# Performance work log

Hardware: AMD Instinct MI355X
Metric: run time of the kernel (lower is better)

The kernel has to match this reference:

```python
import jax, jax.numpy as jnp
import numpy as np

P = 2; NH = 16; HS = 1024; NL = 12; NC = 1000
B, D, H, W = 32, 64, 32, 32
LFEAT = P * P * D  # 256 per-patch feature dim


def _sincos_1d(dim, pos):
    omega = np.arange(dim // 2, dtype=np.float64) / (dim / 2.0)
    omega = 1.0 / 10000 ** omega
    out = np.einsum('m,d->md', pos.reshape(-1), omega)
    return np.concatenate([np.sin(out), np.cos(out)], axis=1)


def _pos_embed(dim, grid_size):
    g = np.arange(grid_size, dtype=np.float32)
    grid = np.stack(np.meshgrid(g, g), axis=0).reshape(2, 1, grid_size, grid_size)
    emb = np.concatenate([_sincos_1d(dim // 2, grid[0]), _sincos_1d(dim // 2, grid[1])], axis=1)
    return jnp.asarray(emb, dtype=jnp.float32)


def setup_inputs() -> dict:
    key = jax.random.key(0)
    ks = iter(jax.random.split(key, 40))
    def w(shape, s=0.02):
        return jax.random.normal(next(ks), shape, jnp.float32) * s
    return {
        'x': jax.random.normal(next(ks), (B, D, H, W), jnp.float32),
        'y': jax.random.randint(next(ks), (B,), 0, NC),
        't': jax.random.randint(next(ks), (B,), 0, 1000),
        'proj_w': w((LFEAT, HS)), 'proj_b': jnp.zeros((HS,), jnp.float32),
        'pos_embed': _pos_embed(HS, H // P),
        'emb_table': w((NC + 1, HS)),
        'blk_mod_w': w((NL, HS, 6 * HS)), 'blk_mod_b': jnp.zeros((NL, 6 * HS), jnp.float32),
        'blk_wq': w((NL, HS, HS)), 'blk_bq': jnp.zeros((NL, HS), jnp.float32),
        'blk_wk': w((NL, HS, HS)), 'blk_bk': jnp.zeros((NL, HS), jnp.float32),
        'blk_wv': w((NL, HS, HS)), 'blk_bv': jnp.zeros((NL, HS), jnp.float32),
        'blk_wo': w((NL, HS, HS)), 'blk_bo': jnp.zeros((NL, HS), jnp.float32),
        'blk_fc1_w': w((NL, HS, 4 * HS)), 'blk_fc1_b': jnp.zeros((NL, 4 * HS), jnp.float32),
        'blk_fc2_w': w((NL, 4 * HS, HS)), 'blk_fc2_b': jnp.zeros((NL, HS), jnp.float32),
        'fin_mod_w': w((HS, 2 * HS)), 'fin_mod_b': jnp.zeros((2 * HS,), jnp.float32),
        'fin_out_w': w((HS, LFEAT)), 'fin_out_b': jnp.zeros((LFEAT,), jnp.float32),
    }


def _ln(z):
    mu = jnp.mean(z, -1, keepdims=True)
    var = jnp.mean((z - mu) ** 2, -1, keepdims=True)
    return (z - mu) * jax.lax.rsqrt(var + 1e-5)


def _forward(x, y, t, proj_w, proj_b, pos_embed, emb_table,
             blk_mod_w, blk_mod_b, blk_wq, blk_bq, blk_wk, blk_bk, blk_wv, blk_bv,
             blk_wo, blk_bo, blk_fc1_w, blk_fc1_b, blk_fc2_w, blk_fc2_b,
             fin_mod_w, fin_mod_b, fin_out_w, fin_out_b):
    Bc, Dc, Hc, Wc = x.shape
    Hp, Wp = Hc // P, Wc // P
    dh = HS // NH
    # patchify_flatten: (B, L, P*P*D)
    tok = x.reshape(Bc, Dc, Hp, P, Wp, P).transpose(0, 2, 4, 3, 5, 1).reshape(Bc, Hp * Wp, P * P * Dc)
    tok = tok @ proj_w + proj_b + pos_embed[None]
    # timestep_embedding: [cos, sin] order per source
    half = HS // 2
    freqs = jnp.exp(-jnp.log(jnp.float32(10000.0)) * jnp.arange(half, dtype=jnp.float32) / half)
    ang = t.astype(jnp.float32)[:, None] * freqs[None]
    c = jnp.concatenate([jnp.cos(ang), jnp.sin(ang)], axis=-1) + emb_table[y]
    c_act = jax.nn.silu(c)  # each block applies silu to c (c is not mutated across blocks)

    def block(xc, p):
        mw, mb, wq, bq, wk, bk, wv, bv, wo, bo, f1w, f1b, f2w, f2b = p
        mod = c_act @ mw + mb
        sh_a, sc_a, g_a, sh_m, sc_m, g_m = jnp.split(mod, 6, axis=1)
        hx = _ln(xc) * (1 + sc_a[:, None]) + sh_a[:, None]
        def heads(z, wz, bz):
            return (z @ wz + bz).reshape(Bc, -1, NH, dh).transpose(0, 2, 1, 3)
        q, k, v = heads(hx, wq, bq), heads(hx, wk, bk), heads(hx, wv, bv)
        logits = jnp.einsum('bhqd,bhkd->bhqk', q, k) / jnp.sqrt(jnp.float32(dh))
        # non-AR mask buffer is all zeros -> no-op
        attn = jax.nn.softmax(logits, axis=-1)
        o = jnp.einsum('bhqk,bhkd->bhqd', attn, v).transpose(0, 2, 1, 3).reshape(Bc, -1, HS)
        xc = xc + g_a[:, None] * (o @ wo + bo)
        hx = _ln(xc) * (1 + sc_m[:, None]) + sh_m[:, None]
        mlp = jax.nn.gelu(hx @ f1w + f1b, approximate=False) @ f2w + f2b
        return xc + g_m[:, None] * mlp, None

    tok, _ = jax.lax.scan(block, tok, (blk_mod_w, blk_mod_b, blk_wq, blk_bq, blk_wk, blk_bk,
                                       blk_wv, blk_bv, blk_wo, blk_bo,
                                       blk_fc1_w, blk_fc1_b, blk_fc2_w, blk_fc2_b))
    fmod = c_act @ fin_mod_w + fin_mod_b
    sh, sc = jnp.split(fmod, 2, axis=1)
    out = (_ln(tok) * (1 + sc[:, None]) + sh[:, None]) @ fin_out_w + fin_out_b
    # unpatchify -> (B, D, H, W)
    return out.reshape(Bc, Hp, Wp, P, P, Dc).transpose(0, 5, 1, 3, 2, 4).reshape(Bc, Dc, Hc, Wc)


def reference(x, y, t, proj_w, proj_b, pos_embed, emb_table,
              blk_mod_w, blk_mod_b, blk_wq, blk_bq, blk_wk, blk_bk, blk_wv, blk_bv,
              blk_wo, blk_bo, blk_fc1_w, blk_fc1_b, blk_fc2_w, blk_fc2_b,
              fin_mod_w, fin_mod_b, fin_out_w, fin_out_b):
    return _forward(x, y, t, proj_w, proj_b, pos_embed, emb_table,
                    blk_mod_w, blk_mod_b, blk_wq, blk_bq, blk_wk, blk_bk, blk_wv, blk_bv,
                    blk_wo, blk_bo, blk_fc1_w, blk_fc1_b, blk_fc2_w, blk_fc2_b,
                    fin_mod_w, fin_mod_b, fin_out_w, fin_out_b)
```

## Files before the change

kernel.cpp:

```cpp
#include <hip/hip_runtime.h>
#include <hip/hip_bf16.h>
#include <math.h>

typedef short s16x8 __attribute__((ext_vector_type(8)));
typedef float f32x4 __attribute__((ext_vector_type(4)));
typedef unsigned short u16;

__device__ __forceinline__ u16 f2b(float f) {
    unsigned u = __builtin_bit_cast(unsigned, f);
    u += 0x7fffu + ((u >> 16) & 1u);
    return (u16)(u >> 16);
}
__device__ __forceinline__ f32x4 mfma16(s16x8 a, s16x8 b, f32x4 c) {
    return __builtin_amdgcn_mfma_f32_16x16x32_bf16(a, b, c, 0, 0, 0);
}
__device__ __forceinline__ void gload16(const void* g, void* l) {
    __builtin_amdgcn_global_load_lds((const __attribute__((address_space(1))) unsigned*)g,
                                     (__attribute__((address_space(3))) unsigned*)l, 16, 0, 0);
}

__global__ __launch_bounds__(256) void patchify_kernel(const float* __restrict__ x, u16* __restrict__ out) {
    int idx = blockIdx.x * 256 + threadIdx.x;
    int row = idx >> 8, col = idx & 255;
    int b = row >> 8, ll = row & 255, hp = ll >> 4, wp = ll & 15;
    int pp = col >> 6, d = col & 63;
    out[idx] = f2b(x[(size_t)((b * 64 + d) * 32 + hp * 2 + (pp >> 1)) * 32 + wp * 2 + (pp & 1)]);
}

__global__ __launch_bounds__(256) void cact_kernel(const int* __restrict__ t, const int* __restrict__ y,
                                                   const float* __restrict__ emb, float* __restrict__ cactF) {
    int b = blockIdx.x, tid = threadIdx.x;
    float tv = (float)t[b];
    int yb = y[b];
#pragma unroll
    for (int j = 0; j < 4; ++j) {
        int c = tid * 4 + j;
        int f = (c < 512) ? c : c - 512;
        float freq = __expf(-9.210340371976184f * (float)f * (1.f / 512.f));
        float ang = tv * freq;
        float v = (c < 512) ? cosf(ang) : sinf(ang);
        v += emb[(size_t)yb * 1024 + c];
        v = v / (1.f + __expf(-v));
        cactF[b * 1024 + c] = v;
    }
}

__global__ __launch_bounds__(256) void bcat_kernel(const float* __restrict__ bq, const float* __restrict__ bk,
                                                   const float* __restrict__ bv, float* __restrict__ out) {
    int lyr = blockIdx.x, j = blockIdx.y, tid = threadIdx.x;
    const float* src = (j == 0) ? bq : ((j == 1) ? bk : bv);
    float4 v = ((const float4*)(src + (size_t)lyr * 1024))[tid];
    ((float4*)(out + (size_t)lyr * 3072 + j * 1024))[tid] = v;
}

__global__ __launch_bounds__(256) void mod32_kernel(const float* __restrict__ cactF, const float* __restrict__ W,
                                                    const float* __restrict__ bias, float* __restrict__ out, int N) {
    __shared__ float cs[32 * 256];
    __shared__ float red[4 * 32 * 64];
    int tid = threadIdx.x, lane = tid & 63, kg = tid >> 6;
    int n = blockIdx.x * 64 + lane;
    float acc[32];
#pragma unroll
    for (int r = 0; r < 32; ++r) acc[r] = 0.f;
    for (int ch = 0; ch < 4; ++ch) {
        __syncthreads();
#pragma unroll
        for (int j = 0; j < 8; ++j) {
            int idx = tid * 4 + j * 1024;
            float4 v = *(const float4*)&cactF[(size_t)(idx >> 8) * 1024 + ch * 256 + (idx & 255)];
            *(float4*)&cs[idx] = v;
        }
        __syncthreads();
        const float* Wp = W + (size_t)(ch * 256 + kg * 64) * N + n;
        for (int kk = 0; kk < 64; kk += 4) {
            float w0 = Wp[(size_t)(kk + 0) * N];
            float w1 = Wp[(size_t)(kk + 1) * N];
            float w2 = Wp[(size_t)(kk + 2) * N];
            float w3 = Wp[(size_t)(kk + 3) * N];
            int kb = kg * 64 + kk;
#pragma unroll
            for (int r = 0; r < 32; ++r) {
                float4 cv = *(const float4*)&cs[r * 256 + kb];
                acc[r] += cv.x * w0 + cv.y * w1 + cv.z * w2 + cv.w * w3;
            }
        }
    }
#pragma unroll
    for (int r = 0; r < 32; ++r) red[(kg * 32 + r) * 64 + lane] = acc[r];
    __syncthreads();
    int r = tid >> 3, j0 = (tid & 7) * 8;
#pragma unroll
    for (int jj = 0; jj < 8; ++jj) {
        int nn = j0 + jj;
        float s = red[(0 * 32 + r) * 64 + nn] + red[(1 * 32 + r) * 64 + nn] +
                  red[(2 * 32 + r) * 64 + nn] + red[(3 * 32 + r) * 64 + nn];
        out[(size_t)r * N + blockIdx.x * 64 + nn] = s + bias[blockIdx.x * 64 + nn];
    }
}

__device__ __forceinline__ void tpose_body(float (*tile)[65], const float* __restrict__ in,
                                           u16* __restrict__ out, int R, int C, int r0, int c0, int tid) {
    int rr = tid >> 4, cc = (tid & 15) * 4;
#pragma unroll
    for (int j = 0; j < 4; ++j) {
        float4 v = *(const float4*)&in[(size_t)(r0 + j * 16 + rr) * C + c0 + cc];
        tile[j * 16 + rr][cc]     = v.x;
        tile[j * 16 + rr][cc + 1] = v.y;
        tile[j * 16 + rr][cc + 2] = v.z;
        tile[j * 16 + rr][cc + 3] = v.w;
    }
    __syncthreads();
    int oc = tid >> 3, r8 = (tid & 7) * 8;
#pragma unroll
    for (int j = 0; j < 2; ++j) {
        int ocl = j * 32 + oc;
        s16x8 vv;
#pragma unroll
        for (int e = 0; e < 8; ++e) vv[e] = (short)f2b(tile[r8 + e][ocl]);
        *(s16x8*)&out[(size_t)(c0 + ocl) * R + r0 + r8] = vv;
    }
}

__global__ __launch_bounds__(256) void transpose_cvt64k(const float* __restrict__ in, u16* __restrict__ out,
                                                        int R, int C) {
    __shared__ float tile[64][65];
    tpose_body(tile, in, out, R, C, blockIdx.y * 64, blockIdx.x * 64, threadIdx.x);
}

__global__ __launch_bounds__(256) void transpose_layer(
    const float* __restrict__ wq, const float* __restrict__ wk,
    const float* __restrict__ wv, const float* __restrict__ wo, const float* __restrict__ f1,
    const float* __restrict__ f2,
    u16* __restrict__ qkvT, u16* __restrict__ woT, u16* __restrict__ f1T, u16* __restrict__ f2T) {
    __shared__ float tile[64][65];
    int bid = blockIdx.x, tid = threadIdx.x;
    const float* src; u16* dst; int R, C, tloc;
    if (bid < 256)       { src = wq; dst = qkvT;               R = 1024; C = 1024; tloc = bid; }
    else if (bid < 512)  { src = wk; dst = qkvT + 1024 * 1024; R = 1024; C = 1024; tloc = bid - 256; }
    else if (bid < 768)  { src = wv; dst = qkvT + 2048 * 1024; R = 1024; C = 1024; tloc = bid - 512; }
    else if (bid < 1024) { src = wo; dst = woT;                R = 1024; C = 1024; tloc = bid - 768; }
    else if (bid < 2048) { src = f1; dst = f1T;                R = 1024; C = 4096; tloc = bid - 1024; }
    else                 { src = f2; dst = f2T;                R = 4096; C = 1024; tloc = bid - 2048; }
    int tx = C >> 6;
    int ty = tloc / tx, txi = tloc - ty * tx;
    tpose_body(tile, src, dst, R, C, ty * 64, txi * 64, tid);
}

__global__ __launch_bounds__(256) void ln_mod_kernel(const float* __restrict__ x, const float* __restrict__ modv,
                                                     int mod_ld, int sh_off, int sc_off, u16* __restrict__ out) {
    int row = blockIdx.x, tid = threadIdx.x, b = row >> 8;
    float4 xv = ((const float4*)(x + (size_t)row * 1024))[tid];
    float s = xv.x + xv.y + xv.z + xv.w;
    float s2 = xv.x * xv.x + xv.y * xv.y + xv.z * xv.z + xv.w * xv.w;
#pragma unroll
    for (int d = 1; d < 64; d <<= 1) { s += __shfl_xor(s, d); s2 += __shfl_xor(s2, d); }
    __shared__ float red[8];
    int w = tid >> 6;
    if ((tid & 63) == 0) { red[w] = s; red[4 + w] = s2; }
    __syncthreads();
    s = red[0] + red[1] + red[2] + red[3];
    s2 = red[4] + red[5] + red[6] + red[7];
    float mu = s * (1.f / 1024.f);
    float rs = rsqrtf(s2 * (1.f / 1024.f) - mu * mu + 1e-5f);
    const float* shp = modv + (size_t)b * mod_ld + sh_off;
    const float* scp = modv + (size_t)b * mod_ld + sc_off;
    float4 sh4 = ((const float4*)shp)[tid];
    float4 sc4 = ((const float4*)scp)[tid];
    u16 o0 = f2b((xv.x - mu) * rs * (1.f + sc4.x) + sh4.x);
    u16 o1 = f2b((xv.y - mu) * rs * (1.f + sc4.y) + sh4.y);
    u16 o2 = f2b((xv.z - mu) * rs * (1.f + sc4.z) + sh4.z);
    u16 o3 = f2b((xv.w - mu) * rs * (1.f + sc4.w) + sh4.w);
    unsigned long long pk = (unsigned long long)o0 | ((unsigned long long)o1 << 16) |
                            ((unsigned long long)o2 << 32) | ((unsigned long long)o3 << 48);
    *(unsigned long long*)&out[(size_t)row * 1024 + tid * 4] = pk;
}

template <int EPI>
__global__ __launch_bounds__(512, 1) void gemm256(
    const u16* __restrict__ A, int lda, const u16* __restrict__ Bt, int ldb,
    int M, int N, int K, const float* __restrict__ bias, u16* __restrict__ outB, int ldc) {
    __shared__ u16 As[3][256 * 32];
    __shared__ u16 Bs[3][256 * 32];

    const int tid = threadIdx.x, w = tid >> 6, l = tid & 63;
    const int wm = w >> 1, wn = w & 1;
    const int fr = l & 15, fg = l >> 4;

    const int nbn = N >> 8;
    const int orig = blockIdx.x;
    const int cpx = gridDim.x >> 3;
    const int wg = (orig & 7) * cpx + (orig >> 3);
    const int bm = wg / nbn, bn = wg - bm * nbn;
    const int row0 = bm << 8, col0 = bn << 8;
    const int NT = K >> 5;

    const int srow = tid >> 2, slot = tid & 3;
    const int gs = slot ^ ((srow >> 1) & 3);
    const u16* gA = A + (size_t)(row0 + srow) * lda + gs * 8;
    const u16* gB = Bt + (size_t)(col0 + srow) * ldb + gs * 8;

    int aoff[4], boff[8];
#pragma unroll
    for (int m = 0; m < 4; ++m) {
        int rr = wm * 64 + m * 16 + fr;
        aoff[m] = rr * 32 + ((fg ^ ((rr >> 1) & 3)) * 8);
    }
#pragma unroll
    for (int j = 0; j < 8; ++j) {
        int rr = wn * 128 + j * 16 + fr;
        boff[j] = rr * 32 + ((fg ^ ((rr >> 1) & 3)) * 8);
    }

    f32x4 acc[4][8];
#pragma unroll
    for (int m = 0; m < 4; ++m)
#pragma unroll
        for (int j = 0; j < 8; ++j) acc[m][j] = (f32x4){0.f, 0.f, 0.f, 0.f};

    {
        u16* d0 = &As[0][tid * 8];
        gload16(gA, d0); gload16(gA + (size_t)128 * lda, d0 + 4096);
        u16* e0 = &Bs[0][tid * 8];
        gload16(gB, e0); gload16(gB + (size_t)128 * ldb, e0 + 4096);
        u16* d1 = &As[1][tid * 8];
        gload16(gA + 32, d1); gload16(gA + (size_t)128 * lda + 32, d1 + 4096);
        u16* e1 = &Bs[1][tid * 8];
        gload16(gB + 32, e1); gload16(gB + (size_t)128 * ldb + 32, e1 + 4096);
    }
    asm volatile("s_waitcnt vmcnt(4)" ::: "memory");
    __builtin_amdgcn_s_barrier();
    __builtin_amdgcn_sched_barrier(0);

    int q = 0;
    for (int t = 0; t < NT; ++t) {
        const u16* ca = As[q];
        const u16* cb = Bs[q];
        const int q1 = (q == 2) ? 0 : q + 1;
        const int q2 = (q1 == 2) ? 0 : q1 + 1;

        s16x8 af[4], bfv[4];
#pragma unroll
        for (int m = 0; m < 4; ++m) af[m] = *(const s16x8*)(ca + aoff[m]);
#pragma unroll
        for (int j = 0; j < 4; ++j) bfv[j] = *(const s16x8*)(cb + boff[j]);
        if (t + 2 < NT) {
            u16* d = &As[q2][tid * 8];
            const u16* s = gA + (size_t)(t + 2) * 32;
            gload16(s, d); gload16(s + (size_t)128 * lda, d + 4096);
        }
        __builtin_amdgcn_s_barrier();
        __builtin_amdgcn_s_setprio(1);
#pragma unroll
        for (int m = 0; m < 4; ++m)
#pragma unroll
            for (int j = 0; j < 4; ++j) acc[m][j] = mfma16(af[m], bfv[j], acc[m][j]);
        __builtin_amdgcn_s_setprio(0);
        __builtin_amdgcn_s_barrier();
#pragma unroll
        for (int j = 0; j < 4; ++j) bfv[j] = *(const s16x8*)(cb + boff[j + 4]);
        if (t + 2 < NT) {
            u16* d = &Bs[q2][tid * 8];
            const u16* s = gB + (size_t)(t + 2) * 32;
            gload16(s, d); gload16(s + (size_t)128 * ldb, d + 4096);
        }
        __builtin_amdgcn_s_setprio(1);
#pragma unroll
        for (int m = 0; m < 4; ++m)
#pragma unroll
            for (int j = 0; j < 4; ++j) acc[m][j + 4] = mfma16(af[m], bfv[j], acc[m][j + 4]);
        __builtin_amdgcn_s_setprio(0);
        if (t < NT - 2)       { asm volatile("s_waitcnt vmcnt(4)" ::: "memory"); }
        else if (t == NT - 2) { asm volatile("s_waitcnt vmcnt(0)" ::: "memory"); }
        if (t < NT - 1) {
            __builtin_amdgcn_s_barrier();
            __builtin_amdgcn_sched_barrier(0);
        }
        q = q1;
    }

    const int erow = row0 + wm * 64 + fg * 4;
    const int ecol = col0 + wn * 128 + fr;
#pragma unroll
    for (int m = 0; m < 4; ++m) {
#pragma unroll
        for (int j = 0; j < 8; ++j) {
#pragma unroll
            for (int r = 0; r < 4; ++r) {
                int row = erow + m * 16 + r;
                int col = ecol + j * 16;
                float v = acc[m][j][r] + bias[col];
                if constexpr (EPI == 1) {
                    outB[(size_t)row * ldc + col] = f2b(v);
                } else {
                    outB[(size_t)row * ldc + col] = f2b(0.5f * v * (1.f + erff(v * 0.70710678118654752f)));
                }
            }
        }
    }
}

template <int EPI>
__global__ __launch_bounds__(512, 1) void gemm8(
    const u16* __restrict__ A, int lda, const u16* __restrict__ Bt, int ldb,
    int M, int N, int K, const float* __restrict__ bias,
    float* __restrict__ outF, u16* __restrict__ outB, int ldc,
    const float* __restrict__ aux1, const float* __restrict__ aux2, int gateOff) {
    __shared__ u16 As[3][256 * 64];
    __shared__ u16 Bs[3][128 * 64];

    const int tid = threadIdx.x, w = tid >> 6, l = tid & 63;
    const int wm = w >> 1, wn = w & 1;

    const int nbn = N >> 7;
    const int orig = blockIdx.x;
    const int cpx = gridDim.x >> 3;
    const int wg = (orig & 7) * cpx + (orig >> 3);
    const int bm = wg / nbn, bn = wg - bm * nbn;
    const int row0 = bm << 8, col0 = bn << 7;

    const int NT = K >> 6;

    const int srow = tid >> 3, sslot = tid & 7;
    const int ksl = sslot ^ (srow & 7);
    const u16* gA = A + (size_t)(row0 + srow) * lda + ksl * 8;
    const u16* gB = Bt + (size_t)(col0 + srow) * ldb + ksl * 8;
    const int lOff = srow * 64 + sslot * 8;

    const int fr = l & 15, fg = l >> 4;
    const int arow = wm * 64 + fr;
    const int brow = wn * 64 + fr;

    f32x4 acc[4][4];
#pragma unroll
    for (int m = 0; m < 4; ++m)
#pragma unroll
        for (int n = 0; n < 4; ++n) acc[m][n] = (f32x4){0.f, 0.f, 0.f, 0.f};

    {
        u16* a0 = &As[0][lOff];
        u16* b0 = &Bs[0][lOff];
#pragma unroll
        for (int a = 0; a < 4; ++a) gload16(gA + (size_t)a * 64 * lda, a0 + a * 4096);
#pragma unroll
        for (int b = 0; b < 2; ++b) gload16(gB + (size_t)b * 64 * ldb, b0 + b * 4096);
        if (NT > 1) {
            u16* a1 = &As[1][lOff];
#pragma unroll
            for (int a = 0; a < 3; ++a) gload16(gA + (size_t)a * 64 * lda + 64, a1 + a * 4096);
        }
    }
    if (NT > 1) { asm volatile("s_waitcnt vmcnt(3)" ::: "memory"); }
    else        { asm volatile("s_waitcnt vmcnt(0)" ::: "memory"); }
    __builtin_amdgcn_s_barrier();
    __builtin_amdgcn_sched_barrier(0);

    int q = 0;
    for (int t = 0; t < NT; ++t) {
        const u16* ca = As[q];
        const u16* cb = Bs[q];
        const int q1 = (q == 2) ? 0 : q + 1;
        const int q2 = (q1 == 2) ? 0 : q1 + 1;

        s16x8 af[4][2], bf[4][2];
#pragma unroll
        for (int m = 0; m < 4; ++m) {
            int r = arow + m * 16;
            af[m][0] = *(const s16x8*)(ca + r * 64 + ((fg     ^ (r & 7)) * 8));
            af[m][1] = *(const s16x8*)(ca + r * 64 + (((4 + fg) ^ (r & 7)) * 8));
        }
#pragma unroll
        for (int n = 0; n < 2; ++n) {
            int r = brow + n * 16;
            bf[n][0] = *(const s16x8*)(cb + r * 64 + ((fg     ^ (r & 7)) * 8));
            bf[n][1] = *(const s16x8*)(cb + r * 64 + (((4 + fg) ^ (r & 7)) * 8));
        }
        if (t + 1 < NT) {
            gload16(gA + (size_t)(3 * 64) * lda + (size_t)(t + 1) * 64, &As[q1][lOff] + 3 * 4096);
            gload16(gB + (size_t)(t + 1) * 64, &Bs[q1][lOff]);
            gload16(gB + (size_t)(1 * 64) * ldb + (size_t)(t + 1) * 64, &Bs[q1][lOff] + 4096);
        }
        __builtin_amdgcn_s_barrier();
        __builtin_amdgcn_s_setprio(1);
#pragma unroll
        for (int m = 0; m < 4; ++m)
#pragma unroll
            for (int n = 0; n < 2; ++n) {
                acc[m][n] = mfma16(af[m][0], bf[n][0], acc[m][n]);
                acc[m][n] = mfma16(af[m][1], bf[n][1], acc[m][n]);
            }
        __builtin_amdgcn_s_setprio(0);
        __builtin_amdgcn_s_barrier();
#pragma unroll
        for (int n = 0; n < 2; ++n) {
            int r = brow + (n + 2) * 16;
            bf[n + 2][0] = *(const s16x8*)(cb + r * 64 + ((fg     ^ (r & 7)) * 8));
            bf[n + 2][1] = *(const s16x8*)(cb + r * 64 + (((4 + fg) ^ (r & 7)) * 8));
        }
        if (t + 2 < NT) {
#pragma unroll
            for (int a = 0; a < 3; ++a)
                gload16(gA + (size_t)a * 64 * lda + (size_t)(t + 2) * 64, &As[q2][lOff] + a * 4096);
        }
        __builtin_amdgcn_s_barrier();
        __builtin_amdgcn_s_setprio(1);
#pragma unroll
        for (int m = 0; m < 4; ++m)
#pragma unroll
            for (int n = 2; n < 4; ++n) {
                acc[m][n] = mfma16(af[m][0], bf[n][0], acc[m][n]);
                acc[m][n] = mfma16(af[m][1], bf[n][1], acc[m][n]);
            }
        __builtin_amdgcn_s_setprio(0);
        if (t < NT - 2)       { asm volatile("s_waitcnt vmcnt(3)" ::: "memory"); }
        else if (t == NT - 2) { asm volatile("s_waitcnt vmcnt(0)" ::: "memory"); }
        if (t < NT - 1) {
            __builtin_amdgcn_s_barrier();
            __builtin_amdgcn_sched_barrier(0);
        }
        q = q1;
    }

    const int erow = row0 + wm * 64 + fg * 4;
    const int ecol = col0 + wn * 64 + fr;
#pragma unroll
    for (int m = 0; m < 4; ++m) {
#pragma unroll
        for (int n = 0; n < 4; ++n) {
#pragma unroll
            for (int r = 0; r < 4; ++r) {
                int row = erow + m * 16 + r;
                int col = ecol + n * 16;
                float v = acc[m][n][r];
                if constexpr (EPI == 2) {
                    outF[(size_t)row * ldc + col] = v + bias[col] + aux1[(size_t)(row & 255) * 1024 + col];
                } else {
                    outF[(size_t)row * ldc + col] =
                        aux1[(size_t)row * ldc + col] +
                        aux2[(size_t)(row >> 8) * 6144 + gateOff + col] * (v + bias[col]);
                }
            }
        }
    }
}

__global__ __launch_bounds__(256, 2) void gemm_fin(
    const u16* __restrict__ A, int lda, const u16* __restrict__ Bt, int ldb,
    int M, int N, int K, const float* __restrict__ bias, float* outF) {
    __shared__ u16 Asl[128 * 32];
    __shared__ u16 Bsl[128 * 32];
    const int tid = threadIdx.x, w = tid >> 6, l = tid & 63;
    const int row0 = blockIdx.y * 128, col0 = blockIdx.x * 128;
    const int wm = w >> 1, wn = w & 1;

    f32x4 acc[4][4];
#pragma unroll
    for (int m = 0; m < 4; ++m)
#pragma unroll
        for (int n = 0; n < 4; ++n) acc[m][n] = (f32x4){0.f, 0.f, 0.f, 0.f};

    const int rA0 = w * 16 + (l >> 2), rA1 = rA0 + 64;
    const int kc = (l & 3) * 8;
    const u16* a0 = A + (size_t)(row0 + rA0) * lda + kc;
    const u16* a1 = A + (size_t)(row0 + rA1) * lda + kc;
    const u16* b0 = Bt + (size_t)(col0 + rA0) * ldb + kc;
    const u16* b1 = Bt + (size_t)(col0 + rA1) * ldb + kc;
    u16* la0 = &Asl[rA0 * 32 + kc];
    u16* la1 = &Asl[rA1 * 32 + kc];
    u16* lb0 = &Bsl[rA0 * 32 + kc];
    u16* lb1 = &Bsl[rA1 * 32 + kc];

    for (int k0 = 0; k0 < K; k0 += 32) {
        __syncthreads();
        gload16(a0 + k0, la0);
        gload16(a1 + k0, la1);
        gload16(b0 + k0, lb0);
        gload16(b1 + k0, lb1);
        __syncthreads();
        s16x8 af[4], bfr[4];
#pragma unroll
        for (int m = 0; m < 4; ++m)
            af[m] = *(const s16x8*)&Asl[(wm * 64 + m * 16 + (l & 15)) * 32 + (l >> 4) * 8];
#pragma unroll
        for (int n = 0; n < 4; ++n)
            bfr[n] = *(const s16x8*)&Bsl[(wn * 64 + n * 16 + (l & 15)) * 32 + (l >> 4) * 8];
#pragma unroll
        for (int m = 0; m < 4; ++m)
#pragma unroll
            for (int n = 0; n < 4; ++n) acc[m][n] = mfma16(af[m], bfr[n], acc[m][n]);
    }

#pragma unroll
    for (int m = 0; m < 4; ++m) {
#pragma unroll
        for (int n = 0; n < 4; ++n) {
#pragma unroll
            for (int r = 0; r < 4; ++r) {
                int row = row0 + wm * 64 + m * 16 + (l >> 4) * 4 + r;
                int col = col0 + wn * 64 + n * 16 + (l & 15);
                float xg = acc[m][n][r] + bias[col];
                int bb = row >> 8, ll = row & 255, hp = ll >> 4, wp = ll & 15;
                int pp = col >> 6, d = col & 63;
                outF[(size_t)((bb * 64 + d) * 32 + hp * 2 + (pp >> 1)) * 32 + wp * 2 + (pp & 1)] = xg;
            }
        }
    }
}

__global__ __launch_bounds__(256, 2) void attn_kernel(const u16* __restrict__ qkv, u16* __restrict__ obuf) {
    __shared__ u16 Qs[64 * 64];
    __shared__ u16 Ks[256 * 64];
    __shared__ u16 VTs[64 * 256];
    int qt = blockIdx.x, h = blockIdx.y, b = blockIdx.z;
    int tid = threadIdx.x, w = tid >> 6, l = tid & 63;
    size_t base = (size_t)b * 256 * 3072;

    {
        int r = tid >> 2;
#pragma unroll
        for (int j = 0; j < 2; ++j) {
            int sg = (tid & 3) + j * 4;
            *(s16x8*)&Qs[r * 64 + sg * 8] =
                *(const s16x8*)&qkv[base + (size_t)(qt * 64 + r) * 3072 + h * 64 + sg * 8];
        }
    }
#pragma unroll
    for (int j = 0; j < 8; ++j) {
        int i = tid + j * 256;
        int r = i >> 3, sg = i & 7;
        *(s16x8*)&Ks[r * 64 + sg * 8] =
            *(const s16x8*)&qkv[base + (size_t)r * 3072 + 1024 + h * 64 + sg * 8];
    }
#pragma unroll
    for (int j = 0; j < 8; ++j) {
        int i = tid + j * 256;
        int r = i >> 3, sg = i & 7;
        s16x8 v = *(const s16x8*)&qkv[base + (size_t)r * 3072 + 2048 + h * 64 + sg * 8];
#pragma unroll
        for (int e = 0; e < 8; ++e) VTs[(sg * 8 + e) * 256 + r] = ((const u16*)&v)[e];
    }
    __syncthreads();

    s16x8 aq0 = *(const s16x8*)&Qs[(w * 16 + (l & 15)) * 64 + (l >> 4) * 8];
    s16x8 aq1 = *(const s16x8*)&Qs[(w * 16 + (l & 15)) * 64 + 32 + (l >> 4) * 8];
    f32x4 sf[16];
#pragma unroll
    for (int cf = 0; cf < 16; ++cf) {
        f32x4 a = (f32x4){0.f, 0.f, 0.f, 0.f};
        s16x8 bk0 = *(const s16x8*)&Ks[(cf * 16 + (l & 15)) * 64 + (l >> 4) * 8];
        s16x8 bk1 = *(const s16x8*)&Ks[(cf * 16 + (l & 15)) * 64 + 32 + (l >> 4) * 8];
        a = mfma16(aq0, bk0, a);
        a = mfma16(aq1, bk1, a);
        sf[cf] = a * 0.125f;
    }
    __syncthreads();

#pragma unroll
    for (int r = 0; r < 4; ++r) {
        float m = -1e30f;
#pragma unroll
        for (int cf = 0; cf < 16; ++cf) m = fmaxf(m, sf[cf][r]);
#pragma unroll
        for (int d = 1; d < 16; d <<= 1) m = fmaxf(m, __shfl_xor(m, d));
        float sm = 0.f;
#pragma unroll
        for (int cf = 0; cf < 16; ++cf) { float e = __expf(sf[cf][r] - m); sf[cf][r] = e; sm += e; }
#pragma unroll
        for (int d = 1; d < 16; d <<= 1) sm += __shfl_xor(sm, d);
        float inv = 1.f / sm;
        int rl = w * 16 + (l >> 4) * 4 + r;
#pragma unroll
        for (int cf = 0; cf < 16; ++cf) Ks[rl * 256 + cf * 16 + (l & 15)] = f2b(sf[cf][r] * inv);
    }
    __syncthreads();

    f32x4 oacc[4];
#pragma unroll
    for (int cf = 0; cf < 4; ++cf) oacc[cf] = (f32x4){0.f, 0.f, 0.f, 0.f};
#pragma unroll
    for (int ks = 0; ks < 8; ++ks) {
        s16x8 ap = *(const s16x8*)&Ks[(w * 16 + (l & 15)) * 256 + ks * 32 + (l >> 4) * 8];
#pragma unroll
        for (int cf = 0; cf < 4; ++cf) {
            s16x8 bv = *(const s16x8*)&VTs[(cf * 16 + (l & 15)) * 256 + ks * 32 + (l >> 4) * 8];
            oacc[cf] = mfma16(ap, bv, oacc[cf]);
        }
    }
    size_t orow0 = (size_t)(b * 256 + qt * 64 + w * 16);
#pragma unroll
    for (int cf = 0; cf < 4; ++cf)
#pragma unroll
        for (int r = 0; r < 4; ++r) {
            int rr = (l >> 4) * 4 + r;
            obuf[(orow0 + rr) * 1024 + h * 64 + cf * 16 + (l & 15)] = f2b(oacc[cf][r]);
        }
}

extern "C" void kernel_launch(void* const* d_in, const int* in_sizes, int n_in,
                              void* d_out, int out_size, void* d_ws, size_t ws_size,
                              hipStream_t stream) {
    (void)in_sizes; (void)n_in; (void)out_size; (void)ws_size;
    const float* x         = (const float*)d_in[0];
    const int*   y         = (const int*)d_in[1];
    const int*   t         = (const int*)d_in[2];
    const float* proj_w    = (const float*)d_in[3];
    const float* proj_b    = (const float*)d_in[4];
    const float* pos_embed = (const float*)d_in[5];
    const float* emb_table = (const float*)d_in[6];
    const float* blk_mod_w = (const float*)d_in[7];
    const float* blk_mod_b = (const float*)d_in[8];
    const float* blk_wq    = (const float*)d_in[9];
    const float* blk_bq    = (const float*)d_in[10];
    const float* blk_wk    = (const float*)d_in[11];
    const float* blk_bk    = (const float*)d_in[12];
    const float* blk_wv    = (const float*)d_in[13];
    const float* blk_bv    = (const float*)d_in[14];
    const float* blk_wo    = (const float*)d_in[15];
    const float* blk_bo    = (const float*)d_in[16];
    const float* blk_f1w   = (const float*)d_in[17];
    const float* blk_f1b   = (const float*)d_in[18];
    const float* blk_f2w   = (const float*)d_in[19];
    const float* blk_f2b   = (const float*)d_in[20];
    const float* fin_mod_w = (const float*)d_in[21];
    const float* fin_mod_b = (const float*)d_in[22];
    const float* fin_out_w = (const float*)d_in[23];
    const float* fin_out_b = (const float*)d_in[24];
    float* out = (float*)d_out;

    char* ws = (char*)d_ws;
    size_t off = 0;
    auto alloc = [&](size_t bytes) -> char* {
        char* p = ws + off;
        off += (bytes + 255) & ~(size_t)255;
        return p;
    };
    float* xc    = (float*)alloc(8192ull * 1024 * 4);
    u16*   hx    = (u16*)alloc(8192ull * 1024 * 2);
    u16*   qkvb  = (u16*)alloc(8192ull * 3072 * 2);
    u16*   obufp = (u16*)alloc(8192ull * 1024 * 2);
    u16*   h1    = (u16*)alloc(8192ull * 4096 * 2);
    u16*   patchA= (u16*)alloc(8192ull * 256 * 2);
    float* cactF = (float*)alloc(32ull * 1024 * 4);
    float* modb  = (float*)alloc(32ull * 6144 * 4);
    float* fmod  = (float*)alloc(32ull * 2048 * 4);
    float* bqkv  = (float*)alloc(12ull * 3072 * 4);
    u16*   projT = (u16*)alloc(1024ull * 256 * 2);
    u16*   foT   = (u16*)alloc(256ull * 1024 * 2);
    u16*   qkvT  = (u16*)alloc(3072ull * 1024 * 2);
    u16*   woT   = (u16*)alloc(1024ull * 1024 * 2);
    u16*   f1T   = (u16*)alloc(4096ull * 1024 * 2);
    u16*   f2T   = (u16*)alloc(1024ull * 4096 * 2);

    patchify_kernel<<<8192, 256, 0, stream>>>(x, patchA);
    cact_kernel<<<32, 256, 0, stream>>>(t, y, emb_table, cactF);
    bcat_kernel<<<dim3(12, 3), 256, 0, stream>>>(blk_bq, blk_bk, blk_bv, bqkv);
    transpose_cvt64k<<<dim3(16, 4), 256, 0, stream>>>(proj_w, projT, 256, 1024);
    transpose_cvt64k<<<dim3(4, 16), 256, 0, stream>>>(fin_out_w, foT, 1024, 256);
    mod32_kernel<<<32, 256, 0, stream>>>(cactF, fin_mod_w, fin_mod_b, fmod, 2048);

    gemm8<2><<<256, 512, 0, stream>>>(patchA, 256, projT, 256, 8192, 1024, 256,
                                      proj_b, xc, nullptr, 1024, pos_embed, nullptr, 0);

    for (int i = 0; i < 12; ++i) {
        transpose_layer<<<3072, 256, 0, stream>>>(
            blk_wq + (size_t)i * 1024 * 1024, blk_wk + (size_t)i * 1024 * 1024,
            blk_wv + (size_t)i * 1024 * 1024, blk_wo + (size_t)i * 1024 * 1024,
            blk_f1w + (size_t)i * 1024 * 4096, blk_f2w + (size_t)i * 4096 * 1024,
            qkvT, woT, f1T, f2T);

        mod32_kernel<<<96, 256, 0, stream>>>(cactF, blk_mod_w + (size_t)i * 1024 * 6144,
                                             blk_mod_b + (size_t)i * 6144, modb, 6144);
        ln_mod_kernel<<<8192, 256, 0, stream>>>(xc, modb, 6144, 0, 1024, hx);
        gemm256<1><<<384, 512, 0, stream>>>(hx, 1024, qkvT, 1024, 8192, 3072, 1024,
                                            bqkv + (size_t)i * 3072, qkvb, 3072);
        attn_kernel<<<dim3(4, 16, 32), 256, 0, stream>>>(qkvb, obufp);
        gemm8<3><<<256, 512, 0, stream>>>(obufp, 1024, woT, 1024, 8192, 1024, 1024,
                                          blk_bo + (size_t)i * 1024, xc, nullptr, 1024,
                                          xc, modb, 2048);
        ln_mod_kernel<<<8192, 256, 0, stream>>>(xc, modb, 6144, 3072, 4096, hx);
        gemm256<4><<<512, 512, 0, stream>>>(hx, 1024, f1T, 1024, 8192, 4096, 1024,
                                            blk_f1b + (size_t)i * 4096, h1, 4096);
        gemm8<3><<<256, 512, 0, stream>>>(h1, 4096, f2T, 4096, 8192, 1024, 4096,
                                          blk_f2b + (size_t)i * 1024, xc, nullptr, 1024,
                                          xc, modb, 5120);
    }
    ln_mod_kernel<<<8192, 256, 0, stream>>>(xc, fmod, 2048, 0, 1024, hx);
    gemm_fin<<<dim3(2, 64), 256, 0, stream>>>(hx, 1024, foT, 1024, 8192, 256, 1024,
                                              fin_out_b, out);
}
```

Baseline: 6.159 ms.

## Rewrite 256x256 GEMM as 8-phase pipeline with BK=64 and double buffering

```diff
diff --git a/kernel.cpp b/kernel.cpp
--- a/kernel.cpp
+++ b/kernel.cpp
@@ -5,6 +5,12 @@
 typedef short s16x8 __attribute__((ext_vector_type(8)));
 typedef float f32x4 __attribute__((ext_vector_type(4)));
 typedef unsigned short u16;
+
+#define BAR() __builtin_amdgcn_s_barrier()
+#define PRIO1() __builtin_amdgcn_s_setprio(1)
+#define PRIO0() __builtin_amdgcn_s_setprio(0)
+#define VMCNT6() asm volatile("s_waitcnt vmcnt(6)" ::: "memory")
+#define VMCNT0() asm volatile("s_waitcnt vmcnt(0)" ::: "memory")
 
 __device__ __forceinline__ u16 f2b(float f) {
     unsigned u = __builtin_bit_cast(unsigned, f);
@@ -176,14 +182,14 @@
 }
 
 template <int EPI>
-__global__ __launch_bounds__(512, 1) void gemm256(
+__global__ __launch_bounds__(512, 2) void gemm256_8ph(
     const u16* __restrict__ A, int lda, const u16* __restrict__ Bt, int ldb,
     int M, int N, int K, const float* __restrict__ bias, u16* __restrict__ outB, int ldc) {
-    __shared__ u16 As[3][256 * 32];
-    __shared__ u16 Bs[3][256 * 32];
+    __shared__ u16 As[2][2][128 * 64];
+    __shared__ u16 Bs[2][2][128 * 64];
 
     const int tid = threadIdx.x, w = tid >> 6, l = tid & 63;
-    const int wm = w >> 1, wn = w & 1;
+    const int wm = w >> 2, wn = w & 3;
     const int fr = l & 15, fg = l >> 4;
 
     const int nbn = N >> 8;
@@ -192,103 +198,108 @@
     const int wg = (orig & 7) * cpx + (orig >> 3);
     const int bm = wg / nbn, bn = wg - bm * nbn;
     const int row0 = bm << 8, col0 = bn << 8;
-    const int NT = K >> 5;
-
-    const int srow = tid >> 2, slot = tid & 3;
-    const int gs = slot ^ ((srow >> 1) & 3);
-    const u16* gA = A + (size_t)(row0 + srow) * lda + gs * 8;
-    const u16* gB = Bt + (size_t)(col0 + srow) * ldb + gs * 8;
-
-    int aoff[4], boff[8];
-#pragma unroll
-    for (int m = 0; m < 4; ++m) {
-        int rr = wm * 64 + m * 16 + fr;
-        aoff[m] = rr * 32 + ((fg ^ ((rr >> 1) & 3)) * 8);
-    }
-#pragma unroll
-    for (int j = 0; j < 8; ++j) {
-        int rr = wn * 128 + j * 16 + fr;
-        boff[j] = rr * 32 + ((fg ^ ((rr >> 1) & 3)) * 8);
-    }
-
-    f32x4 acc[4][8];
-#pragma unroll
-    for (int m = 0; m < 4; ++m)
-#pragma unroll
-        for (int j = 0; j < 8; ++j) acc[m][j] = (f32x4){0.f, 0.f, 0.f, 0.f};
-
-    {
-        u16* d0 = &As[0][tid * 8];
-        gload16(gA, d0); gload16(gA + (size_t)128 * lda, d0 + 4096);
-        u16* e0 = &Bs[0][tid * 8];
-        gload16(gB, e0); gload16(gB + (size_t)128 * ldb, e0 + 4096);
-        u16* d1 = &As[1][tid * 8];
-        gload16(gA + 32, d1); gload16(gA + (size_t)128 * lda + 32, d1 + 4096);
-        u16* e1 = &Bs[1][tid * 8];
-        gload16(gB + 32, e1); gload16(gB + (size_t)128 * ldb + 32, e1 + 4096);
-    }
-    asm volatile("s_waitcnt vmcnt(4)" ::: "memory");
-    __builtin_amdgcn_s_barrier();
+    const int NT = K >> 6;
+
+    const int srow = tid >> 3, slot = tid & 7;
+    const int gsl = slot ^ (srow & 7);
+
+    auto stA = [&](int d, int h, int tt) {
+        const u16* src = A + (size_t)(row0 + h * 128 + srow) * lda + (size_t)tt * 64 + gsl * 8;
+        u16* dst = &As[d][h][tid * 8];
+        gload16(src, dst);
+        gload16(src + (size_t)64 * lda, dst + 64 * 64);
+    };
+    auto stB = [&](int d, int h, int tt) {
+        const u16* src = Bt + (size_t)(col0 + h * 128 + srow) * ldb + (size_t)tt * 64 + gsl * 8;
+        u16* dst = &Bs[d][h][tid * 8];
+        gload16(src, dst);
+        gload16(src + (size_t)64 * ldb, dst + 64 * 64);
+    };
+
+    const int swz0 = (fg ^ (fr & 7)) * 8;
+    const int swz1 = ((fg + 4) ^ (fr & 7)) * 8;
+    auto ldA = [&](int d, int mh, s16x8 (&out)[4][2]) {
+#pragma unroll
+        for (int m = 0; m < 4; ++m) {
+            const u16* p = &As[d][wm][(mh * 64 + m * 16 + fr) * 64];
+            out[m][0] = *(const s16x8*)(p + swz0);
+            out[m][1] = *(const s16x8*)(p + swz1);
+        }
+    };
+    auto ldB = [&](int d, int nh, s16x8 (&out)[2][2]) {
+#pragma unroll
+        for (int n = 0; n < 2; ++n) {
+            const u16* p = &Bs[d][wn >> 1][((wn & 1) * 64 + nh * 32 + n * 16 + fr) * 64];
+            out[n][0] = *(const s16x8*)(p + swz0);
+            out[n][1] = *(const s16x8*)(p + swz1);
+        }
+    };
+
+    f32x4 acc[8][4];
+#pragma unroll
+    for (int m = 0; m < 8; ++m)
+#pragma unroll
+        for (int n = 0; n < 4; ++n) acc[m][n] = (f32x4){0.f, 0.f, 0.f, 0.f};
+
+    auto MQ = [&](int mh, int nh, s16x8 (&Aa)[4][2], s16x8 (&Bb)[2][2]) {
+#pragma unroll
+        for (int m = 0; m < 4; ++m)
+#pragma unroll
+            for (int n = 0; n < 2; ++n) {
+                f32x4 c = acc[mh * 4 + m][nh * 2 + n];
+                c = mfma16(Aa[m][0], Bb[n][0], c);
+                c = mfma16(Aa[m][1], Bb[n][1], c);
+                acc[mh * 4 + m][nh * 2 + n] = c;
+            }
+    };
+
+    stA(0, 0, 0); stA(0, 1, 0); stB(0, 0, 0); stB(0, 1, 0);
+    stA(1, 0, 1); stA(1, 1, 1); stB(1, 0, 1);
+    VMCNT6();
+    BAR();
     __builtin_amdgcn_sched_barrier(0);
 
-    int q = 0;
-    for (int t = 0; t < NT; ++t) {
-        const u16* ca = As[q];
-        const u16* cb = Bs[q];
-        const int q1 = (q == 2) ? 0 : q + 1;
-        const int q2 = (q1 == 2) ? 0 : q1 + 1;
-
-        s16x8 af[4], bfv[4];
-#pragma unroll
-        for (int m = 0; m < 4; ++m) af[m] = *(const s16x8*)(ca + aoff[m]);
-#pragma unroll
-        for (int j = 0; j < 4; ++j) bfv[j] = *(const s16x8*)(cb + boff[j]);
-        if (t + 2 < NT) {
-            u16* d = &As[q2][tid * 8];
-            const u16* s = gA + (size_t)(t + 2) * 32;
-            gload16(s, d); gload16(s + (size_t)128 * lda, d + 4096);
-        }
-        __builtin_amdgcn_s_barrier();
-        __builtin_amdgcn_s_setprio(1);
-#pragma unroll
-        for (int m = 0; m < 4; ++m)
-#pragma unroll
-            for (int j = 0; j < 4; ++j) acc[m][j] = mfma16(af[m], bfv[j], acc[m][j]);
-        __builtin_amdgcn_s_setprio(0);
-        __builtin_amdgcn_s_barrier();
-#pragma unroll
-        for (int j = 0; j < 4; ++j) bfv[j] = *(const s16x8*)(cb + boff[j + 4]);
-        if (t + 2 < NT) {
-            u16* d = &Bs[q2][tid * 8];
-            const u16* s = gB + (size_t)(t + 2) * 32;
-            gload16(s, d); gload16(s + (size_t)128 * ldb, d + 4096);
-        }
-        __builtin_amdgcn_s_setprio(1);
-#pragma unroll
-        for (int m = 0; m < 4; ++m)
-#pragma unroll
-            for (int j = 0; j < 4; ++j) acc[m][j + 4] = mfma16(af[m], bfv[j], acc[m][j + 4]);
-        __builtin_amdgcn_s_setprio(0);
-        if (t < NT - 2)       { asm volatile("s_waitcnt vmcnt(4)" ::: "memory"); }
-        else if (t == NT - 2) { asm volatile("s_waitcnt vmcnt(0)" ::: "memory"); }
-        if (t < NT - 1) {
-            __builtin_amdgcn_s_barrier();
+    for (int t = 0; t < NT; t += 2) {
+        const bool more = (t + 2 < NT);
+        s16x8 Aa[4][2], Ab[4][2], B0[2][2], B1[2][2];
+        ldA(0, 0, Aa); ldB(0, 0, B0);
+        stB(1, 1, t + 1);
+        BAR(); PRIO1(); MQ(0, 0, Aa, B0); PRIO0(); BAR();
+        ldB(0, 1, B1);
+        BAR(); PRIO1(); MQ(0, 1, Aa, B1); PRIO0(); BAR();
+        ldA(0, 1, Ab);
+        if (more) stB(0, 0, t + 2);
+        BAR(); PRIO1(); MQ(1, 1, Ab, B1); PRIO0(); BAR();
+        if (more) { stB(0, 1, t + 2); stA(0, 0, t + 2); }
+        BAR(); PRIO1(); MQ(1, 0, Ab, B0); PRIO0();
+        if (more) { VMCNT6(); } else { VMCNT0(); }
+        BAR();
+        ldA(1, 0, Aa); ldB(1, 0, B0);
+        if (more) stA(0, 1, t + 2);
+        BAR(); PRIO1(); MQ(0, 0, Aa, B0); PRIO0(); BAR();
+        ldB(1, 1, B1);
+        BAR(); PRIO1(); MQ(0, 1, Aa, B1); PRIO0(); BAR();
+        ldA(1, 1, Ab);
+        if (more) stB(1, 0, t + 3);
+        BAR(); PRIO1(); MQ(1, 1, Ab, B1); PRIO0(); BAR();
+        if (more) { stA(1, 0, t + 3); stA(1, 1, t + 3); }
+        BAR(); PRIO1(); MQ(1, 0, Ab, B0); PRIO0();
+        if (more) {
+            VMCNT6();
+            BAR();
             __builtin_amdgcn_sched_barrier(0);
         }
-        q = q1;
-    }
-
-    const int erow = row0 + wm * 64 + fg * 4;
-    const int ecol = col0 + wn * 128 + fr;
-#pragma unroll
-    for (int m = 0; m < 4; ++m) {
-#pragma unroll
-        for (int j = 0; j < 8; ++j) {
+    }
+
+#pragma unroll
+    for (int m = 0; m < 8; ++m) {
+#pragma unroll
+        for (int n = 0; n < 4; ++n) {
 #pragma unroll
             for (int r = 0; r < 4; ++r) {
-                int row = erow + m * 16 + r;
-                int col = ecol + j * 16;
-                float v = acc[m][j][r] + bias[col];
+                int row = row0 + wm * 128 + m * 16 + fg * 4 + r;
+                int col = col0 + wn * 64 + n * 16 + fr;
+                float v = acc[m][n][r] + bias[col];
                 if constexpr (EPI == 1) {
                     outB[(size_t)row * ldc + col] = f2b(v);
                 } else {
@@ -350,8 +361,8 @@
         }
     }
     if (NT > 1) { asm volatile("s_waitcnt vmcnt(3)" ::: "memory"); }
-    else        { asm volatile("s_waitcnt vmcnt(0)" ::: "memory"); }
-    __builtin_amdgcn_s_barrier();
+    else        { VMCNT0(); }
+    BAR();
     __builtin_amdgcn_sched_barrier(0);
 
     int q = 0;
@@ -379,8 +390,7 @@
             gload16(gB + (size_t)(t + 1) * 64, &Bs[q1][lOff]);
             gload16(gB + (size_t)(1 * 64) * ldb + (size_t)(t + 1) * 64, &Bs[q1][lOff] + 4096);
         }
-        __builtin_amdgcn_s_barrier();
-        __builtin_amdgcn_s_setprio(1);
+        BAR(); PRIO1();
 #pragma unroll
         for (int m = 0; m < 4; ++m)
 #pragma unroll
@@ -388,8 +398,7 @@
                 acc[m][n] = mfma16(af[m][0], bf[n][0], acc[m][n]);
                 acc[m][n] = mfma16(af[m][1], bf[n][1], acc[m][n]);
             }
-        __builtin_amdgcn_s_setprio(0);
-        __builtin_amdgcn_s_barrier();
+        PRIO0(); BAR();
 #pragma unroll
         for (int n = 0; n < 2; ++n) {
             int r = brow + (n + 2) * 16;
@@ -401,8 +410,7 @@
             for (int a = 0; a < 3; ++a)
                 gload16(gA + (size_t)a * 64 * lda + (size_t)(t + 2) * 64, &As[q2][lOff] + a * 4096);
         }
-        __builtin_amdgcn_s_barrier();
-        __builtin_amdgcn_s_setprio(1);
+        BAR(); PRIO1();
 #pragma unroll
         for (int m = 0; m < 4; ++m)
 #pragma unroll
@@ -410,11 +418,11 @@
                 acc[m][n] = mfma16(af[m][0], bf[n][0], acc[m][n]);
                 acc[m][n] = mfma16(af[m][1], bf[n][1], acc[m][n]);
             }
-        __builtin_amdgcn_s_setprio(0);
+        PRIO0();
         if (t < NT - 2)       { asm volatile("s_waitcnt vmcnt(3)" ::: "memory"); }
-        else if (t == NT - 2) { asm volatile("s_waitcnt vmcnt(0)" ::: "memory"); }
+        else if (t == NT - 2) { VMCNT0(); }
         if (t < NT - 1) {
-            __builtin_amdgcn_s_barrier();
+            BAR();
             __builtin_amdgcn_sched_barrier(0);
         }
         q = q1;
@@ -670,15 +678,15 @@
         mod32_kernel<<<96, 256, 0, stream>>>(cactF, blk_mod_w + (size_t)i * 1024 * 6144,
                                              blk_mod_b + (size_t)i * 6144, modb, 6144);
         ln_mod_kernel<<<8192, 256, 0, stream>>>(xc, modb, 6144, 0, 1024, hx);
-        gemm256<1><<<384, 512, 0, stream>>>(hx, 1024, qkvT, 1024, 8192, 3072, 1024,
-                                            bqkv + (size_t)i * 3072, qkvb, 3072);
+        gemm256_8ph<1><<<384, 512, 0, stream>>>(hx, 1024, qkvT, 1024, 8192, 3072, 1024,
+                                                bqkv + (size_t)i * 3072, qkvb, 3072);
         attn_kernel<<<dim3(4, 16, 32), 256, 0, stream>>>(qkvb, obufp);
         gemm8<3><<<256, 512, 0, stream>>>(obufp, 1024, woT, 1024, 8192, 1024, 1024,
                                           blk_bo + (size_t)i * 1024, xc, nullptr, 1024,
                                           xc, modb, 2048);
         ln_mod_kernel<<<8192, 256, 0, stream>>>(xc, modb, 6144, 3072, 4096, hx);
-        gemm256<4><<<512, 512, 0, stream>>>(hx, 1024, f1T, 1024, 8192, 4096, 1024,
-                                            blk_f1b + (size_t)i * 4096, h1, 4096);
+        gemm256_8ph<4><<<512, 512, 0, stream>>>(hx, 1024, f1T, 1024, 8192, 4096, 1024,
+                                                blk_f1b + (size_t)i * 4096, h1, 4096);
         gemm8<3><<<256, 512, 0, stream>>>(h1, 4096, f2T, 4096, 8192, 1024, 4096,
                                           blk_f2b + (size_t)i * 1024, xc, nullptr, 1024,
                                           xc, modb, 5120);
```

After: 6.092 ms. About the same (-1.1%).
